# Performance work log

Hardware: AMD Instinct MI355X
Metric: run time of the kernel (lower is better)

The kernel has to match this reference:

```python
import jax, jax.numpy as jnp
import numpy as np
from jax import lax

B, T, D, K = 2, 4096, 128, 256


def setup_inputs() -> dict:
    key = jax.random.key(0)
    ks = jax.random.split(key, 5)
    s = 0.05
    return {
        "z": jax.random.normal(ks[0], (B, T, D), jnp.float32),
        "conv_kernel": jax.random.normal(ks[1], (K, 1, D), jnp.float32) * s,  # flax WIO depthwise
        "conv_bias": jnp.zeros((D,), jnp.float32),
        "Wq": jax.random.normal(ks[2], (D, D), jnp.float32) * s,
        "bq": jnp.zeros((D,), jnp.float32),
        "Wk": jax.random.normal(ks[3], (D, D), jnp.float32) * s,
        "bk": jnp.zeros((D,), jnp.float32),
        "Wo": jax.random.normal(ks[4], (D, D), jnp.float32) * s,
        "bo": jnp.zeros((D,), jnp.float32),
    }


def _sphere_norm(x):
    return x / jnp.maximum(jnp.linalg.norm(x, axis=-1, keepdims=True), 1e-8)


def reference(z, conv_kernel, conv_bias, Wq, bq, Wk, bk, Wo, bo):
    Bv, Tv, Dv = z.shape
    Kv = conv_kernel.shape[0]

    # Depthwise causal memory conv (flax nn.Conv, padding='CAUSAL', groups=D)
    memory_force = lax.conv_general_dilated(
        z, conv_kernel, window_strides=(1,), padding=[(Kv - 1, 0)],
        dimension_numbers=("NWC", "WIO", "NWC"), feature_group_count=Dv,
    ) + conv_bias

    # Keys are computed from the base point z once, shared across RK4 stages
    k_hat = _sphere_norm(z @ Wk + bk)  # [B,T,D]
    mask = jnp.tril(jnp.ones((Tv, Tv), z.dtype))  # causal mask

    def vector_field(z_curr):
        q_hat = _sphere_norm(z_curr @ Wq + bq)
        dots = jnp.einsum("btd,bsd->bts", q_hat, k_hat)  # [B,T,T]
        attn = jnp.sin(dots) * mask  # Kuramoto-style sin coupling, causal
        kuramoto = jnp.einsum("bts,bsd->btd", attn, k_hat) @ Wo + bo
        total = memory_force + kuramoto
        # project to tangent space of the sphere at z_curr
        return total - jnp.sum(total * z_curr, axis=-1, keepdims=True) * z_curr

    h = 1.0

    def retract(z_base, v):
        return _sphere_norm(z_base + v)

    k1 = vector_field(z)
    k2 = vector_field(retract(z, 0.5 * h * k1))
    k3 = vector_field(retract(z, 0.5 * h * k2))
    k4 = vector_field(retract(z, h * k3))
    v_final = (h / 6.0) * (k1 + 2 * k2 + 2 * k3 + k4)
    return retract(z, v_final)
```

## Files before the change

### kernel.cpp

```cpp
#include <hip/hip_runtime.h>
#include <hip/hip_bf16.h>

#define BB 2
#define TT 4096
#define DD 128
#define KK 256
#define NROW (BB*TT)
#define NELT (NROW*DD)

typedef _Float16 f16;
typedef __attribute__((ext_vector_type(8))) f16 half8;
typedef __attribute__((ext_vector_type(4))) float f32x4;

__global__ __launch_bounds__(256) void k_proj(
    const float* __restrict__ z, const float* __restrict__ Wk, const float* __restrict__ bk,
    f16* __restrict__ khb, f16* __restrict__ khT)
{
  __shared__ float Ws[DD*DD];
  __shared__ float zs[32*DD];
  int tid = threadIdx.x;
  int r0 = blockIdx.x * 32;
  #pragma unroll
  for (int it = 0; it < 16; it++){
    int idx = tid + it*256;
    *(f32x4*)(Ws + idx*4) = *(const f32x4*)(Wk + (size_t)idx*4);
  }
  #pragma unroll
  for (int it = 0; it < 4; it++){
    int idx = tid + it*256;
    *(f32x4*)(zs + idx*4) = *(const f32x4*)(z + (size_t)r0*DD + idx*4);
  }
  __syncthreads();
  int c = tid & 15, rr = tid >> 4;
  float acc0[8], acc1[8];
  #pragma unroll
  for (int u = 0; u < 8; u++){ float bv = bk[c*8+u]; acc0[u] = bv; acc1[u] = bv; }
  const float* zr0 = zs + rr*DD;
  const float* zr1 = zs + (rr+16)*DD;
  #pragma unroll 4
  for (int i = 0; i < DD; i++){
    f32x4 w0 = *(const f32x4*)(Ws + i*DD + c*8);
    f32x4 w1 = *(const f32x4*)(Ws + i*DD + c*8 + 4);
    float a0 = zr0[i], a1 = zr1[i];
    #pragma unroll
    for (int u = 0; u < 4; u++){
      acc0[u]   = fmaf(a0, w0[u], acc0[u]);   acc1[u]   = fmaf(a1, w0[u], acc1[u]);
      acc0[4+u] = fmaf(a0, w1[u], acc0[4+u]); acc1[4+u] = fmaf(a1, w1[u], acc1[4+u]);
    }
  }
  float s0 = 0.f, s1 = 0.f;
  #pragma unroll
  for (int u = 0; u < 8; u++){ s0 = fmaf(acc0[u], acc0[u], s0); s1 = fmaf(acc1[u], acc1[u], s1); }
  #pragma unroll
  for (int m = 1; m < 16; m <<= 1){ s0 += __shfl_xor(s0, m, 16); s1 += __shfl_xor(s1, m, 16); }
  float inv0 = 1.f / fmaxf(sqrtf(s0), 1e-8f);
  float inv1 = 1.f / fmaxf(sqrtf(s1), 1e-8f);
  half8 h0, h1;
  #pragma unroll
  for (int u = 0; u < 8; u++){ h0[u] = (f16)(acc0[u]*inv0); h1[u] = (f16)(acc1[u]*inv1); }
  int row0 = r0 + rr, row1 = row0 + 16;
  *(half8*)(khb + (size_t)row0*DD + c*8) = h0;
  *(half8*)(khb + (size_t)row1*DD + c*8) = h1;
  int b = row0 >> 12, t0 = row0 & 4095, t1 = row1 & 4095;
  #pragma unroll
  for (int u = 0; u < 8; u++){
    khT[((size_t)b*DD + c*8 + u)*TT + t0] = h0[u];
    khT[((size_t)b*DD + c*8 + u)*TT + t1] = h1[u];
  }
}

__global__ __launch_bounds__(256) void k_conv(
    const float* __restrict__ z, const float* __restrict__ ck, const float* __restrict__ cb,
    float* __restrict__ mf)
{
  int tid = threadIdx.x;
  int d = tid & 127, tg = tid >> 7;
  int bid = blockIdx.x;
  int b = bid >> 8;
  int tbase = ((bid & 255) << 4) + tg*8;
  const float* zb = z + (size_t)b*TT*DD;
  float acc[8];
  #pragma unroll
  for (int j = 0; j < 8; j++) acc[j] = 0.f;
  float ckq[8];
  #pragma unroll
  for (int u = 0; u < 8; u++) ckq[u] = 0.f;
  int sstart = tbase - (KK-1);
  for (int ch = 0; ch < 33; ch++){
    #pragma unroll
    for (int u = 0; u < 8; u++){
      int base = ch*8 + u;
      int s = sstart + base;
      float zv = ((unsigned)s < (unsigned)TT && base < 263) ? zb[(size_t)s*DD + d] : 0.f;
      ckq[u] = (base < KK) ? ck[(size_t)base*DD + d] : 0.f;
      #pragma unroll
      for (int j = 0; j < 8; j++) acc[j] = fmaf(ckq[(u-j)&7], zv, acc[j]);
    }
  }
  float cbv = cb[d];
  #pragma unroll
  for (int j = 0; j < 8; j++)
    mf[((size_t)b*TT + tbase + j)*DD + d] = acc[j] + cbv;
}

__global__ __launch_bounds__(256) void k_q(
    const float* __restrict__ zcur, const float* __restrict__ Wq, const float* __restrict__ bq,
    f16* __restrict__ qhb)
{
  __shared__ float Ws[DD*DD];
  __shared__ float zs[32*DD];
  int tid = threadIdx.x;
  int r0 = blockIdx.x * 32;
  #pragma unroll
  for (int it = 0; it < 16; it++){
    int idx = tid + it*256;
    *(f32x4*)(Ws + idx*4) = *(const f32x4*)(Wq + (size_t)idx*4);
  }
  #pragma unroll
  for (int it = 0; it < 4; it++){
    int idx = tid + it*256;
    *(f32x4*)(zs + idx*4) = *(const f32x4*)(zcur + (size_t)r0*DD + idx*4);
  }
  __syncthreads();
  int c = tid & 15, rr = tid >> 4;
  float acc0[8], acc1[8];
  #pragma unroll
  for (int u = 0; u < 8; u++){ float bv = bq[c*8+u]; acc0[u] = bv; acc1[u] = bv; }
  const float* zr0 = zs + rr*DD;
  const float* zr1 = zs + (rr+16)*DD;
  #pragma unroll 4
  for (int i = 0; i < DD; i++){
    f32x4 w0 = *(const f32x4*)(Ws + i*DD + c*8);
    f32x4 w1 = *(const f32x4*)(Ws + i*DD + c*8 + 4);
    float a0 = zr0[i], a1 = zr1[i];
    #pragma unroll
    for (int u = 0; u < 4; u++){
      acc0[u]   = fmaf(a0, w0[u], acc0[u]);   acc1[u]   = fmaf(a1, w0[u], acc1[u]);
      acc0[4+u] = fmaf(a0, w1[u], acc0[4+u]); acc1[4+u] = fmaf(a1, w1[u], acc1[4+u]);
    }
  }
  float s0 = 0.f, s1 = 0.f;
  #pragma unroll
  for (int u = 0; u < 8; u++){ s0 = fmaf(acc0[u], acc0[u], s0); s1 = fmaf(acc1[u], acc1[u], s1); }
  #pragma unroll
  for (int m = 1; m < 16; m <<= 1){ s0 += __shfl_xor(s0, m, 16); s1 += __shfl_xor(s1, m, 16); }
  float inv0 = 1.f / fmaxf(sqrtf(s0), 1e-8f);
  float inv1 = 1.f / fmaxf(sqrtf(s1), 1e-8f);
  half8 h0, h1;
  #pragma unroll
  for (int u = 0; u < 8; u++){ h0[u] = (f16)(acc0[u]*inv0); h1[u] = (f16)(acc1[u]*inv1); }
  *(half8*)(qhb + (size_t)(r0+rr)*DD + c*8) = h0;
  *(half8*)(qhb + (size_t)(r0+rr+16)*DD + c*8) = h1;
}

#define QTILE 128
#define NQT3 (TT/QTILE)
#define NCHUNK 272

__global__ __launch_bounds__(256,2) void k_attn7(
    const f16* __restrict__ qhb, const f16* __restrict__ khb,
    const f16* __restrict__ khT, f16* __restrict__ part)
{
  int bid = blockIdx.x;
  int b = bid / NCHUNK;
  int rem = bid - b*NCHUNK;
  int qt = 0, chunk = 0;
  #pragma unroll 1
  for (int j = 0; j < NQT3; j++){
    int nch = (j + 2) >> 1;
    if (rem < nch){ qt = j; chunk = rem; break; }
    rem -= nch;
  }
  int kt0 = chunk * 4;
  int kt1 = min(kt0 + 3, 2*qt + 1);
  int t0 = qt * QTILE;

  __shared__ __align__(16) f16 Kb[64*136];
  __shared__ __align__(16) f16 Kt[128*72];
  __shared__ __align__(16) f16 Ps[4][32*72];

  int tid  = threadIdx.x;
  int w    = tid >> 6;
  int lane = tid & 63;
  int n16  = lane & 15;
  int g    = lane >> 4;

  const f16* qg  = qhb + (size_t)b*TT*DD;
  const f16* kg  = khb + (size_t)b*TT*DD;
  const f16* ktg = khT + (size_t)b*DD*TT;

  int sb_r  = tid >> 4, sb_c = (tid & 15)*8;
  int st_r  = tid >> 3, st_c = (tid & 7)*8;

  half8 qa[2][4];
  #pragma unroll
  for (int p = 0; p < 2; p++){
    const f16* qrow = qg + (size_t)(t0 + 32*w + 16*p + n16)*DD + g*8;
    #pragma unroll
    for (int c = 0; c < 4; c++) qa[p][c] = *(const half8*)(qrow + 32*c);
  }
  f32x4 acc[2][8];
  #pragma unroll
  for (int p = 0; p < 2; p++)
    #pragma unroll
    for (int i = 0; i < 8; i++) acc[p][i] = (f32x4){0.f,0.f,0.f,0.f};

  f16* psw = &Ps[w][0];

  half8 sKb[4], sKt[4];
  {
    int s0 = kt0 * 64;
    #pragma unroll
    for (int it = 0; it < 4; it++)
      sKb[it] = *(const half8*)(kg + (size_t)(s0 + sb_r + it*16)*DD + sb_c);
    #pragma unroll
    for (int it = 0; it < 4; it++)
      sKt[it] = *(const half8*)(ktg + (size_t)(st_r + it*32)*TT + s0 + st_c);
  }

  for (int kt = kt0; kt <= kt1; kt++){
    #pragma unroll
    for (int it = 0; it < 4; it++)
      *(half8*)(Kb + (sb_r + it*16)*136 + sb_c) = sKb[it];
    #pragma unroll
    for (int it = 0; it < 4; it++)
      *(half8*)(Kt + (st_r + it*32)*72 + st_c) = sKt[it];
    __syncthreads();

    if (kt < kt1){
      int s0n = (kt+1) * 64;
      #pragma unroll
      for (int it = 0; it < 4; it++)
        sKb[it] = *(const half8*)(kg + (size_t)(s0n + sb_r + it*16)*DD + sb_c);
      #pragma unroll
      for (int it = 0; it < 4; it++)
        sKt[it] = *(const half8*)(ktg + (size_t)(st_r + it*32)*TT + s0n + st_c);
    }

    int s0 = kt * 64;
    f32x4 s_acc[2][4];
    #pragma unroll
    for (int p = 0; p < 2; p++)
      #pragma unroll
      for (int n = 0; n < 4; n++) s_acc[p][n] = (f32x4){0.f,0.f,0.f,0.f};
    #pragma unroll
    for (int c = 0; c < 4; c++){
      #pragma unroll
      for (int n = 0; n < 4; n++){
        half8 bf = *(const half8*)(Kb + (16*n + n16)*136 + 32*c + g*8);
        s_acc[0][n] = __builtin_amdgcn_mfma_f32_16x16x32_f16(qa[0][c], bf, s_acc[0][n], 0,0,0);
        s_acc[1][n] = __builtin_amdgcn_mfma_f32_16x16x32_f16(qa[1][c], bf, s_acc[1][n], 0,0,0);
      }
    }
    #pragma unroll
    for (int p = 0; p < 2; p++){
      int qrow = t0 + 32*w + 16*p + 4*g;
      #pragma unroll
      for (int n = 0; n < 4; n++){
        int key = s0 + 16*n + n16;
        #pragma unroll
        for (int r = 0; r < 4; r++){
          float v = (key <= qrow + r) ? __sinf(s_acc[p][n][r]) : 0.f;
          psw[(16*p + 4*g + r)*72 + 16*n + n16] = (f16)v;
        }
      }
    }

    #pragma unroll
    for (int h = 0; h < 2; h++){
      half8 pa[2];
      #pragma unroll
      for (int p = 0; p < 2; p++)
        pa[p] = *(const half8*)(psw + (16*p + n16)*72 + 32*h + 8*g);
      #pragma unroll
      for (int nt = 0; nt < 8; nt++){
        half8 bf = *(const half8*)(Kt + (16*nt + n16)*72 + 32*h + 8*g);
        acc[0][nt] = __builtin_amdgcn_mfma_f32_16x16x32_f16(pa[0], bf, acc[0][nt], 0,0,0);
        acc[1][nt] = __builtin_amdgcn_mfma_f32_16x16x32_f16(pa[1], bf, acc[1][nt], 0,0,0);
      }
    }
    __syncthreads();
  }

  f16* pb = part + (size_t)bid*(QTILE*DD) + (32*w)*DD;
  #pragma unroll
  for (int p = 0; p < 2; p++){
    #pragma unroll
    for (int nt = 0; nt < 8; nt++){
      #pragma unroll
      for (int r = 0; r < 4; r++){
        pb[(size_t)(16*p + 4*g + r)*DD + 16*nt + n16] = (f16)acc[p][nt][r];
      }
    }
  }
}

__global__ __launch_bounds__(256) void k_reduce(
    const f16* __restrict__ part, float* __restrict__ att)
{
  int bid = blockIdx.x;
  int rg = bid & 7;
  int qt = (bid >> 3) & 31;
  int b  = bid >> 8;
  int nc = (qt + 2) >> 1;
  int base = ((qt + 1)*(qt + 1)) >> 2;
  int tid = threadIdx.x;
  size_t off = (size_t)rg*(16*DD) + tid*8;
  const f16* src = part + ((size_t)b*NCHUNK + base)*(QTILE*DD) + off;
  float a[8];
  {
    half8 v = *(const half8*)(src);
    #pragma unroll
    for (int u = 0; u < 8; u++) a[u] = (float)v[u];
  }
  for (int c = 1; c < nc; c++){
    half8 v = *(const half8*)(src + (size_t)c*(QTILE*DD));
    #pragma unroll
    for (int u = 0; u < 8; u++) a[u] += (float)v[u];
  }
  float* dst = att + ((size_t)b*TT + (size_t)qt*QTILE)*DD + off;
  f32x4 o0 = {a[0],a[1],a[2],a[3]}, o1 = {a[4],a[5],a[6],a[7]};
  *(f32x4*)(dst) = o0;
  *(f32x4*)(dst + 4) = o1;
}

__global__ __launch_bounds__(256) void k_comb(
    const float* __restrict__ z, const float* __restrict__ Wo, const float* __restrict__ bo,
    const float* __restrict__ mf, const float* __restrict__ att,
    const float* __restrict__ zin, float* __restrict__ zout,
    float* __restrict__ vsum, float* __restrict__ out,
    float wsum, float cretr, int first, int last)
{
  __shared__ float Ws[DD*DD];
  __shared__ float As[32*DD];
  int tid = threadIdx.x;
  int r0 = blockIdx.x * 32;
  #pragma unroll
  for (int it = 0; it < 16; it++){
    int idx = tid + it*256;
    *(f32x4*)(Ws + idx*4) = *(const f32x4*)(Wo + (size_t)idx*4);
  }
  #pragma unroll
  for (int it = 0; it < 4; it++){
    int idx = tid + it*256;
    *(f32x4*)(As + idx*4) = *(const f32x4*)(att + (size_t)r0*DD + idx*4);
  }
  __syncthreads();
  int c = tid & 15, rr = tid >> 4;
  float kur0[8], kur1[8];
  #pragma unroll
  for (int u = 0; u < 8; u++){ float bv = bo[c*8+u]; kur0[u] = bv; kur1[u] = bv; }
  const float* ar0 = As + rr*DD;
  const float* ar1 = As + (rr+16)*DD;
  #pragma unroll 4
  for (int i = 0; i < DD; i++){
    f32x4 w0 = *(const f32x4*)(Ws + i*DD + c*8);
    f32x4 w1 = *(const f32x4*)(Ws + i*DD + c*8 + 4);
    float a0 = ar0[i], a1 = ar1[i];
    #pragma unroll
    for (int u = 0; u < 4; u++){
      kur0[u]   = fmaf(a0, w0[u], kur0[u]);   kur1[u]   = fmaf(a1, w0[u], kur1[u]);
      kur0[4+u] = fmaf(a0, w1[u], kur0[4+u]); kur1[4+u] = fmaf(a1, w1[u], kur1[4+u]);
    }
  }
  size_t o0 = (size_t)(r0+rr)*DD + c*8;
  size_t o1 = (size_t)(r0+rr+16)*DD + c*8;
  float tot0[8], tot1[8], zi0[8], zi1[8];
  {
    f32x4 m0a = *(const f32x4*)(mf + o0), m0b = *(const f32x4*)(mf + o0 + 4);
    f32x4 m1a = *(const f32x4*)(mf + o1), m1b = *(const f32x4*)(mf + o1 + 4);
    f32x4 z0a = *(const f32x4*)(zin + o0), z0b = *(const f32x4*)(zin + o0 + 4);
    f32x4 z1a = *(const f32x4*)(zin + o1), z1b = *(const f32x4*)(zin + o1 + 4);
    #pragma unroll
    for (int u = 0; u < 4; u++){
      tot0[u] = m0a[u] + kur0[u]; tot0[4+u] = m0b[u] + kur0[4+u];
      tot1[u] = m1a[u] + kur1[u]; tot1[4+u] = m1b[u] + kur1[4+u];
      zi0[u] = z0a[u]; zi0[4+u] = z0b[u];
      zi1[u] = z1a[u]; zi1[4+u] = z1b[u];
    }
  }
  float p0 = 0.f, p1 = 0.f;
  #pragma unroll
  for (int u = 0; u < 8; u++){ p0 = fmaf(tot0[u], zi0[u], p0); p1 = fmaf(tot1[u], zi1[u], p1); }
  #pragma unroll
  for (int m = 1; m < 16; m <<= 1){ p0 += __shfl_xor(p0, m, 16); p1 += __shfl_xor(p1, m, 16); }
  float ki0[8], ki1[8], vs0[8], vs1[8];
  #pragma unroll
  for (int u = 0; u < 8; u++){
    ki0[u] = tot0[u] - p0 * zi0[u];
    ki1[u] = tot1[u] - p1 * zi1[u];
  }
  if (first){
    #pragma unroll
    for (int u = 0; u < 8; u++){ vs0[u] = wsum*ki0[u]; vs1[u] = wsum*ki1[u]; }
  } else {
    f32x4 v0a = *(const f32x4*)(vsum + o0), v0b = *(const f32x4*)(vsum + o0 + 4);
    f32x4 v1a = *(const f32x4*)(vsum + o1), v1b = *(const f32x4*)(vsum + o1 + 4);
    #pragma unroll
    for (int u = 0; u < 4; u++){
      vs0[u] = fmaf(wsum, ki0[u], v0a[u]); vs0[4+u] = fmaf(wsum, ki0[4+u], v0b[u]);
      vs1[u] = fmaf(wsum, ki1[u], v1a[u]); vs1[4+u] = fmaf(wsum, ki1[4+u], v1b[u]);
    }
  }
  if (!last){
    f32x4 va = {vs0[0],vs0[1],vs0[2],vs0[3]}, vb = {vs0[4],vs0[5],vs0[6],vs0[7]};
    f32x4 vc = {vs1[0],vs1[1],vs1[2],vs1[3]}, vd = {vs1[4],vs1[5],vs1[6],vs1[7]};
    *(f32x4*)(vsum + o0) = va; *(f32x4*)(vsum + o0 + 4) = vb;
    *(f32x4*)(vsum + o1) = vc; *(f32x4*)(vsum + o1 + 4) = vd;
  }
  float nz0[8], nz1[8];
  {
    f32x4 z0a = *(const f32x4*)(z + o0), z0b = *(const f32x4*)(z + o0 + 4);
    f32x4 z1a = *(const f32x4*)(z + o1), z1b = *(const f32x4*)(z + o1 + 4);
    #pragma unroll
    for (int u = 0; u < 4; u++){
      float d0a = last ? vs0[u]*(1.f/6.f)   : cretr*ki0[u];
      float d0b = last ? vs0[4+u]*(1.f/6.f) : cretr*ki0[4+u];
      float d1a = last ? vs1[u]*(1.f/6.f)   : cretr*ki1[u];
      float d1b = last ? vs1[4+u]*(1.f/6.f) : cretr*ki1[4+u];
      nz0[u] = z0a[u] + d0a; nz0[4+u] = z0b[u] + d0b;
      nz1[u] = z1a[u] + d1a; nz1[4+u] = z1b[u] + d1b;
    }
  }
  float n0 = 0.f, n1 = 0.f;
  #pragma unroll
  for (int u = 0; u < 8; u++){ n0 = fmaf(nz0[u], nz0[u], n0); n1 = fmaf(nz1[u], nz1[u], n1); }
  #pragma unroll
  for (int m = 1; m < 16; m <<= 1){ n0 += __shfl_xor(n0, m, 16); n1 += __shfl_xor(n1, m, 16); }
  float i0 = 1.f / fmaxf(sqrtf(n0), 1e-8f);
  float i1 = 1.f / fmaxf(sqrtf(n1), 1e-8f);
  float* dst = last ? out : zout;
  f32x4 ra = {nz0[0]*i0, nz0[1]*i0, nz0[2]*i0, nz0[3]*i0};
  f32x4 rb = {nz0[4]*i0, nz0[5]*i0, nz0[6]*i0, nz0[7]*i0};
  f32x4 rc = {nz1[0]*i1, nz1[1]*i1, nz1[2]*i1, nz1[3]*i1};
  f32x4 rd = {nz1[4]*i1, nz1[5]*i1, nz1[6]*i1, nz1[7]*i1};
  *(f32x4*)(dst + o0) = ra; *(f32x4*)(dst + o0 + 4) = rb;
  *(f32x4*)(dst + o1) = rc; *(f32x4*)(dst + o1 + 4) = rd;
}

extern "C" void kernel_launch(void* const* d_in, const int* in_sizes, int n_in,
                              void* d_out, int out_size, void* d_ws, size_t ws_size,
                              hipStream_t stream) {
  const float* z  = (const float*)d_in[0];
  const float* ck = (const float*)d_in[1];
  const float* cb = (const float*)d_in[2];
  const float* Wq = (const float*)d_in[3];
  const float* bq = (const float*)d_in[4];
  const float* Wk = (const float*)d_in[5];
  const float* bk = (const float*)d_in[6];
  const float* Wo = (const float*)d_in[7];
  const float* bo = (const float*)d_in[8];
  float* out = (float*)d_out;

  float* mf   = (float*)d_ws;
  float* zc   = mf   + NELT;
  float* att  = zc   + NELT;
  float* vsum = att  + NELT;
  f16*   khb  = (f16*)(vsum + NELT);
  f16*   khT  = khb  + NELT;
  f16*   qhb  = khT  + NELT;
  f16*   part = qhb  + NELT;

  k_proj<<<NROW/32, 256, 0, stream>>>(z, Wk, bk, khb, khT);
  k_conv<<<BB*TT/16, 256, 0, stream>>>(z, ck, cb, mf);

  const float wv[4] = {1.f, 2.f, 2.f, 1.f};
  const float cv[4] = {0.5f, 0.5f, 1.f, 0.f};
  for (int st = 0; st < 4; st++){
    const float* zcur = (st == 0) ? z : zc;
    k_q     <<<NROW/32, 256, 0, stream>>>(zcur, Wq, bq, qhb);
    k_attn7 <<<BB*NCHUNK, 256, 0, stream>>>(qhb, khb, khT, part);
    k_reduce<<<BB*NQT3*8, 256, 0, stream>>>(part, att);
    k_comb  <<<NROW/32, 256, 0, stream>>>(z, Wo, bo, mf, att, zcur, zc, vsum, out,
                                          wv[st], cv[st], st == 0, st == 3);
  }
}
```

Baseline: 314.3 us.

## Fuse split-K reduction into attention kernel via last-block atomic counter

```diff
diff --git a/kernel.cpp b/kernel.cpp
--- a/kernel.cpp
+++ b/kernel.cpp
@@ -10,7 +10,14 @@
 
 typedef _Float16 f16;
 typedef __attribute__((ext_vector_type(8))) f16 half8;
+typedef __attribute__((ext_vector_type(2))) __fp16 fp16x2;
 typedef __attribute__((ext_vector_type(4))) float f32x4;
+typedef __attribute__((ext_vector_type(2))) int i32x2;
+
+__device__ __forceinline__ int pack2(float a, float b){
+  fp16x2 h = __builtin_amdgcn_cvt_pkrtz(a, b);
+  return __builtin_bit_cast(int, h);
+}
 
 __global__ __launch_bounds__(256) void k_proj(
     const float* __restrict__ z, const float* __restrict__ Wk, const float* __restrict__ bk,
@@ -105,12 +112,13 @@
 
 __global__ __launch_bounds__(256) void k_q(
     const float* __restrict__ zcur, const float* __restrict__ Wq, const float* __restrict__ bq,
-    f16* __restrict__ qhb)
+    f16* __restrict__ qhb, int* __restrict__ cnt)
 {
   __shared__ float Ws[DD*DD];
   __shared__ float zs[32*DD];
   int tid = threadIdx.x;
   int r0 = blockIdx.x * 32;
+  if (blockIdx.x == 0 && tid < 64) cnt[tid] = 0;
   #pragma unroll
   for (int it = 0; it < 16; it++){
     int idx = tid + it*256;
@@ -157,9 +165,10 @@
 #define NQT3 (TT/QTILE)
 #define NCHUNK 272
 
-__global__ __launch_bounds__(256,2) void k_attn7(
+__global__ __launch_bounds__(256,2) void k_attn8(
     const f16* __restrict__ qhb, const f16* __restrict__ khb,
-    const f16* __restrict__ khT, f16* __restrict__ part)
+    const f16* __restrict__ khT, f16* __restrict__ part,
+    float* __restrict__ att, int* __restrict__ cnt)
 {
   int bid = blockIdx.x;
   int b = bid / NCHUNK;
@@ -178,6 +187,7 @@
   __shared__ __align__(16) f16 Kb[64*136];
   __shared__ __align__(16) f16 Kt[128*72];
   __shared__ __align__(16) f16 Ps[4][32*72];
+  __shared__ int lastFlag;
 
   int tid  = threadIdx.x;
   int w    = tid >> 6;
@@ -247,22 +257,23 @@
     for (int c = 0; c < 4; c++){
       #pragma unroll
       for (int n = 0; n < 4; n++){
-        half8 bf = *(const half8*)(Kb + (16*n + n16)*136 + 32*c + g*8);
-        s_acc[0][n] = __builtin_amdgcn_mfma_f32_16x16x32_f16(qa[0][c], bf, s_acc[0][n], 0,0,0);
-        s_acc[1][n] = __builtin_amdgcn_mfma_f32_16x16x32_f16(qa[1][c], bf, s_acc[1][n], 0,0,0);
+        half8 af = *(const half8*)(Kb + (16*n + n16)*136 + 32*c + g*8);
+        s_acc[0][n] = __builtin_amdgcn_mfma_f32_16x16x32_f16(af, qa[0][c], s_acc[0][n], 0,0,0);
+        s_acc[1][n] = __builtin_amdgcn_mfma_f32_16x16x32_f16(af, qa[1][c], s_acc[1][n], 0,0,0);
       }
     }
     #pragma unroll
     for (int p = 0; p < 2; p++){
-      int qrow = t0 + 32*w + 16*p + 4*g;
+      int qrow = t0 + 32*w + 16*p + n16;
       #pragma unroll
       for (int n = 0; n < 4; n++){
-        int key = s0 + 16*n + n16;
-        #pragma unroll
-        for (int r = 0; r < 4; r++){
-          float v = (key <= qrow + r) ? __sinf(s_acc[p][n][r]) : 0.f;
-          psw[(16*p + 4*g + r)*72 + 16*n + n16] = (f16)v;
-        }
+        int keyr = s0 + 16*n + 4*g;
+        float v0 = (keyr     <= qrow) ? __sinf(s_acc[p][n][0]) : 0.f;
+        float v1 = (keyr + 1 <= qrow) ? __sinf(s_acc[p][n][1]) : 0.f;
+        float v2 = (keyr + 2 <= qrow) ? __sinf(s_acc[p][n][2]) : 0.f;
+        float v3 = (keyr + 3 <= qrow) ? __sinf(s_acc[p][n][3]) : 0.f;
+        i32x2 pw = { pack2(v0, v1), pack2(v2, v3) };
+        *(i32x2*)(psw + (16*p + n16)*72 + 16*n + 4*g) = pw;
       }
     }
 
@@ -293,35 +304,36 @@
       }
     }
   }
-}
-
-__global__ __launch_bounds__(256) void k_reduce(
-    const f16* __restrict__ part, float* __restrict__ att)
-{
-  int bid = blockIdx.x;
-  int rg = bid & 7;
-  int qt = (bid >> 3) & 31;
-  int b  = bid >> 8;
-  int nc = (qt + 2) >> 1;
-  int base = ((qt + 1)*(qt + 1)) >> 2;
-  int tid = threadIdx.x;
-  size_t off = (size_t)rg*(16*DD) + tid*8;
-  const f16* src = part + ((size_t)b*NCHUNK + base)*(QTILE*DD) + off;
-  float a[8];
-  {
-    half8 v = *(const half8*)(src);
-    #pragma unroll
-    for (int u = 0; u < 8; u++) a[u] = (float)v[u];
-  }
-  for (int c = 1; c < nc; c++){
-    half8 v = *(const half8*)(src + (size_t)c*(QTILE*DD));
-    #pragma unroll
-    for (int u = 0; u < 8; u++) a[u] += (float)v[u];
-  }
-  float* dst = att + ((size_t)b*TT + (size_t)qt*QTILE)*DD + off;
-  f32x4 o0 = {a[0],a[1],a[2],a[3]}, o1 = {a[4],a[5],a[6],a[7]};
-  *(f32x4*)(dst) = o0;
-  *(f32x4*)(dst + 4) = o1;
+
+  int nAll = (qt + 2) >> 1;
+  __threadfence();
+  __syncthreads();
+  if (tid == 0){
+    int old = atomicAdd(&cnt[b*NQT3 + qt], 1);
+    lastFlag = (old == nAll - 1);
+  }
+  __syncthreads();
+  if (lastFlag){
+    __threadfence();
+    int cbase = ((qt + 1)*(qt + 1)) >> 2;
+    const f16* srcb = part + ((size_t)b*NCHUNK + cbase)*(QTILE*DD);
+    float* dst = att + ((size_t)b*TT + t0)*DD;
+    #pragma unroll 1
+    for (int i = tid; i < QTILE*DD/8; i += 256){
+      float a[8];
+      half8 v = *(const half8*)(srcb + (size_t)i*8);
+      #pragma unroll
+      for (int u = 0; u < 8; u++) a[u] = (float)v[u];
+      for (int cc = 1; cc < nAll; cc++){
+        half8 v2 = *(const half8*)(srcb + (size_t)cc*(QTILE*DD) + (size_t)i*8);
+        #pragma unroll
+        for (int u = 0; u < 8; u++) a[u] += (float)v2[u];
+      }
+      f32x4 o0 = {a[0],a[1],a[2],a[3]}, o1 = {a[4],a[5],a[6],a[7]};
+      *(f32x4*)(dst + (size_t)i*8) = o0;
+      *(f32x4*)(dst + (size_t)i*8 + 4) = o1;
+    }
+  }
 }
 
 __global__ __launch_bounds__(256) void k_comb(
@@ -460,6 +472,7 @@
   f16*   khT  = khb  + NELT;
   f16*   qhb  = khT  + NELT;
   f16*   part = qhb  + NELT;
+  int*   cnt  = (int*)(part + (size_t)BB*NCHUNK*QTILE*DD);
 
   k_proj<<<NROW/32, 256, 0, stream>>>(z, Wk, bk, khb, khT);
   k_conv<<<BB*TT/16, 256, 0, stream>>>(z, ck, cb, mf);
@@ -468,10 +481,9 @@
   const float cv[4] = {0.5f, 0.5f, 1.f, 0.f};
   for (int st = 0; st < 4; st++){
     const float* zcur = (st == 0) ? z : zc;
-    k_q     <<<NROW/32, 256, 0, stream>>>(zcur, Wq, bq, qhb);
-    k_attn7 <<<BB*NCHUNK, 256, 0, stream>>>(qhb, khb, khT, part);
-    k_reduce<<<BB*NQT3*8, 256, 0, stream>>>(part, att);
-    k_comb  <<<NROW/32, 256, 0, stream>>>(z, Wo, bo, mf, att, zcur, zc, vsum, out,
-                                          wv[st], cv[st], st == 0, st == 3);
-  }
-}
+    k_q    <<<NROW/32, 256, 0, stream>>>(zcur, Wq, bq, qhb, cnt);
+    k_attn8<<<BB*NCHUNK, 256, 0, stream>>>(qhb, khb, khT, part, att, cnt);
+    k_comb <<<NROW/32, 256, 0, stream>>>(z, Wo, bo, mf, att, zcur, zc, vsum, out,
+                                         wv[st], cv[st], st == 0, st == 3);
+  }
+}
```

Measured after the change: 762.8 us. 143% more time.
